# Performance work log

Hardware: AMD Instinct MI355X
Metric: run time of the kernel (lower is better)

Reference implementation:

```python
import jax, jax.numpy as jnp
import numpy as np

N_USER = 100000
N_ITEM = 100000
E = 800000
IN_USER, IN_ITEM, HID, OUT = 256, 128, 128, 64


def _gconv(x_src, W, b, src, dst, n_src, n_dst):
    """DGL GraphConv, norm='both', transform-before-aggregate (in>=out here)."""
    ones = jnp.ones(src.shape[0], x_src.dtype)
    deg_out = jax.ops.segment_sum(ones, src, num_segments=n_src)
    deg_in = jax.ops.segment_sum(ones, dst, num_segments=n_dst)
    inv_out = jnp.maximum(deg_out, 1.0) ** -0.5
    inv_in = jnp.maximum(deg_in, 1.0) ** -0.5
    x = (x_src @ W) * inv_out[:, None]            # [n_src, out]
    agg = jax.ops.segment_sum(x[src], dst, num_segments=n_dst)  # scatter-add over edges
    return agg * inv_in[:, None] + b


def setup_inputs() -> dict:
    key = jax.random.key(0)
    ks = jax.random.split(key, 24)
    d = {
        "feat_user": jax.random.normal(ks[0], (N_USER, IN_USER), jnp.float32),
        "feat_item": jax.random.normal(ks[1], (N_ITEM, IN_ITEM), jnp.float32),
        "rates_src": jax.random.randint(ks[2], (E,), 0, N_USER, jnp.int32),
        "rates_dst": jax.random.randint(ks[3], (E,), 0, N_ITEM, jnp.int32),
        "rated_src": jax.random.randint(ks[4], (E,), 0, N_ITEM, jnp.int32),
        "rated_dst": jax.random.randint(ks[5], (E,), 0, N_USER, jnp.int32),
        "fol_src": jax.random.randint(ks[6], (E,), 0, N_USER, jnp.int32),
        "fol_dst": jax.random.randint(ks[7], (E,), 0, N_USER, jnp.int32),
    }
    def glorot(k, shp):
        lim = np.sqrt(6.0 / (shp[0] + shp[1]))
        return jax.random.uniform(k, shp, jnp.float32, -lim, lim)
    d["W1_rates"] = glorot(ks[8], (IN_USER, HID)); d["b1_rates"] = jnp.zeros((HID,), jnp.float32)
    d["W1_rated"] = glorot(ks[9], (IN_ITEM, HID)); d["b1_rated"] = jnp.zeros((HID,), jnp.float32)
    d["W1_fol"] = glorot(ks[10], (IN_USER, HID)); d["b1_fol"] = jnp.zeros((HID,), jnp.float32)
    d["W2_rates"] = glorot(ks[11], (HID, OUT)); d["b2_rates"] = jnp.zeros((OUT,), jnp.float32)
    d["W2_rated"] = glorot(ks[12], (HID, OUT)); d["b2_rated"] = jnp.zeros((OUT,), jnp.float32)
    d["W2_fol"] = glorot(ks[13], (HID, OUT)); d["b2_fol"] = jnp.zeros((OUT,), jnp.float32)
    return d


def reference(feat_user, feat_item, rates_src, rates_dst, rated_src, rated_dst,
              fol_src, fol_dst, W1_rates, b1_rates, W1_rated, b1_rated,
              W1_fol, b1_fol, W2_rates, b2_rates, W2_rated, b2_rated,
              W2_fol, b2_fol):
    # layer 1 (HeteroGraphConv, sum-aggregate across relations per dst ntype)
    h_item = _gconv(feat_user, W1_rates, b1_rates, rates_src, rates_dst, N_USER, N_ITEM)
    h_user = (_gconv(feat_item, W1_rated, b1_rated, rated_src, rated_dst, N_ITEM, N_USER)
              + _gconv(feat_user, W1_fol, b1_fol, fol_src, fol_dst, N_USER, N_USER))
    # relu (dropout = identity in eval mode)
    h_user = jax.nn.relu(h_user)
    h_item = jax.nn.relu(h_item)
    # layer 2
    o_item = _gconv(h_user, W2_rates, b2_rates, rates_src, rates_dst, N_USER, N_ITEM)
    o_user = (_gconv(h_item, W2_rated, b2_rated, rated_src, rated_dst, N_ITEM, N_USER)
              + _gconv(h_user, W2_fol, b2_fol, fol_src, fol_dst, N_USER, N_USER))
    return jnp.stack([o_user, o_item])  # [2, N, OUT]
```

## Files before the change

### kernel.cpp

```cpp
#include <hip/hip_runtime.h>
#include <math.h>

#define IN_USER 256
#define IN_ITEM 128
#define HID 128
#define OUTF 64
#define NRANGE 8
#define NCHUNK 16
#define MAXRB 12544

typedef unsigned short u16;
typedef unsigned int u32;
typedef __attribute__((ext_vector_type(8))) __bf16 bf16x8;
typedef __attribute__((ext_vector_type(4))) float f32x4;

__device__ __forceinline__ u16 f2bf(float f) {
    union { float f; u32 u; } c; c.f = f;
    return (u16)((c.u + 0x7fffu + ((c.u >> 16) & 1u)) >> 16);
}
__device__ __forceinline__ u32 pack2(float a, float b) {
    return (u32)f2bf(a) | ((u32)f2bf(b) << 16);
}

__global__ __launch_bounds__(512) void hist_ranges(
        const int* __restrict__ a0, int e0, const int* __restrict__ a1, int e1,
        const int* __restrict__ a2, int e2, const int* __restrict__ a3, int e3,
        const int* __restrict__ a4, int e4, const int* __restrict__ a5, int e5,
        int* __restrict__ hist, int NP, int RB) {
    __shared__ int h[MAXRB];
    const int a = blockIdx.z;
    const int* arr; int E;
    switch (a) {
        case 0: arr = a0; E = e0; break;
        case 1: arr = a1; E = e1; break;
        case 2: arr = a2; E = e2; break;
        case 3: arr = a3; E = e3; break;
        case 4: arr = a4; E = e4; break;
        default: arr = a5; E = e5; break;
    }
    const int c = blockIdx.y;
    const int lo = blockIdx.x * RB;
    const u32 rbu = (u32)RB;
    const int tid = threadIdx.x;
    for (int i = tid; i < RB; i += 512) h[i] = 0;
    __syncthreads();
    const int ec = (((E + NCHUNK - 1) / NCHUNK) + 3) & ~3;
    const int s0 = c * ec;
    const int s1 = (s0 + ec) < E ? (s0 + ec) : E;
    if (s1 > s0) {
        const int n4 = (s1 - s0) >> 2;
        const int4* p4 = reinterpret_cast<const int4*>(arr + s0);
        for (int i = tid; i < n4; i += 512) {
            const int4 A = p4[i];
            u32 ux = (u32)(A.x - lo); if (ux < rbu) atomicAdd(&h[ux], 1);
            u32 uy = (u32)(A.y - lo); if (uy < rbu) atomicAdd(&h[uy], 1);
            u32 uz = (u32)(A.z - lo); if (uz < rbu) atomicAdd(&h[uz], 1);
            u32 uw = (u32)(A.w - lo); if (uw < rbu) atomicAdd(&h[uw], 1);
        }
        for (int j = s0 + (n4 << 2) + tid; j < s1; j += 512) {
            const u32 u = (u32)(arr[j] - lo);
            if (u < rbu) atomicAdd(&h[u], 1);
        }
    }
    __syncthreads();
    int* out = hist + ((size_t)a * NCHUNK + c) * NP + lo;
    for (int i = tid; i < RB; i += 512) out[i] = h[i];
}

__global__ __launch_bounds__(256) void hist_reduce(
        int* __restrict__ hist, int* __restrict__ deg,
        float* __restrict__ inv, int NP) {
    const int a = blockIdx.y;
    const int v = blockIdx.x * 256 + threadIdx.x;
    if (v >= NP) return;
    int* h = hist + (size_t)a * NCHUNK * NP + v;
    int s = 0;
#pragma unroll
    for (int c = 0; c < NCHUNK; ++c) {
        const int t = h[(size_t)c * NP];
        if (a & 1) h[(size_t)c * NP] = s;
        s += t;
    }
    deg[(size_t)a * NP + v] = s;
    inv[(size_t)a * NP + v] = 1.0f / sqrtf((float)(s > 1 ? s : 1));
}

__global__ __launch_bounds__(256) void scan_part(
        const int* __restrict__ d0, const int* __restrict__ d1,
        const int* __restrict__ d2, int n0, int n1, int n2,
        int* __restrict__ partial, int nblk) {
    const int rel = blockIdx.y;
    const int* deg = rel == 0 ? d0 : (rel == 1 ? d1 : d2);
    const int n = rel == 0 ? n0 : (rel == 1 ? n1 : n2);
    const int base = blockIdx.x * 1024 + threadIdx.x * 4;
    int s = 0;
#pragma unroll
    for (int i = 0; i < 4; ++i) {
        const int idx = base + i;
        if (idx < n) s += deg[idx];
    }
    __shared__ int red[256];
    red[threadIdx.x] = s;
    __syncthreads();
#pragma unroll
    for (int off = 128; off > 0; off >>= 1) {
        if (threadIdx.x < off) red[threadIdx.x] += red[threadIdx.x + off];
        __syncthreads();
    }
    if (threadIdx.x == 0) partial[rel * nblk + blockIdx.x] = red[0];
}

__global__ __launch_bounds__(128) void scan_mid(int* __restrict__ partial, int nblk) {
    __shared__ int sc[128];
    const int rel = blockIdx.x;
    const int t = threadIdx.x;
    const int v = (t < nblk) ? partial[rel * nblk + t] : 0;
    sc[t] = v;
    __syncthreads();
    for (int off = 1; off < 128; off <<= 1) {
        const int u = (t >= off) ? sc[t - off] : 0;
        __syncthreads();
        sc[t] += u;
        __syncthreads();
    }
    if (t < nblk) partial[rel * nblk + t] = sc[t] - v;
}

__global__ __launch_bounds__(256) void scan_final(
        const int* __restrict__ d0, const int* __restrict__ d1,
        const int* __restrict__ d2, int n0, int n1, int n2,
        const int* __restrict__ partial,
        int* __restrict__ c0, int* __restrict__ c1, int* __restrict__ c2,
        int nblk) {
    const int rel = blockIdx.y;
    const int* deg = rel == 0 ? d0 : (rel == 1 ? d1 : d2);
    int* cur = rel == 0 ? c0 : (rel == 1 ? c1 : c2);
    const int n = rel == 0 ? n0 : (rel == 1 ? n1 : n2);
    const int base = blockIdx.x * 1024 + threadIdx.x * 4;
    int v[4];
    int s = 0;
#pragma unroll
    for (int i = 0; i < 4; ++i) {
        const int idx = base + i;
        v[i] = (idx < n) ? deg[idx] : 0;
        s += v[i];
    }
    __shared__ int sc[256];
    sc[threadIdx.x] = s;
    __syncthreads();
    for (int off = 1; off < 256; off <<= 1) {
        const int u = (threadIdx.x >= off) ? sc[threadIdx.x - off] : 0;
        __syncthreads();
        sc[threadIdx.x] += u;
        __syncthreads();
    }
    int run = (threadIdx.x == 0 ? 0 : sc[threadIdx.x - 1]) + partial[rel * nblk + blockIdx.x];
#pragma unroll
    for (int i = 0; i < 4; ++i) {
        const int idx = base + i;
        if (idx < n) cur[idx] = run;
        run += v[i];
    }
}

__global__ __launch_bounds__(512) void fill_ranges(
        const int* __restrict__ s0p, const int* __restrict__ d0p, int e0,
        const int* __restrict__ s1p, const int* __restrict__ d1p, int e1,
        const int* __restrict__ s2p, const int* __restrict__ d2p, int e2,
        const int* __restrict__ cursor, const int* __restrict__ hist,
        int NP, int RB,
        int* __restrict__ csrbase, int off1, int off2) {
    __shared__ int cur[MAXRB];
    const int rel = blockIdx.z;
    const int* src = rel == 0 ? s0p : (rel == 1 ? s1p : s2p);
    const int* dst = rel == 0 ? d0p : (rel == 1 ? d1p : d2p);
    const int E = rel == 0 ? e0 : (rel == 1 ? e1 : e2);
    int* csr = csrbase + (rel == 0 ? 0 : (rel == 1 ? off1 : off2));
    const int c = blockIdx.y;
    const int lo = blockIdx.x * RB;
    const u32 rbu = (u32)RB;
    const int tid = threadIdx.x;
    const int* gc = cursor + (size_t)rel * NP + lo;
    const int* go = hist + ((size_t)(2 * rel + 1) * NCHUNK + c) * NP + lo;
    for (int i = tid; i < RB; i += 512) cur[i] = gc[i] + go[i];
    __syncthreads();
    const int ec = (((E + NCHUNK - 1) / NCHUNK) + 3) & ~3;
    const int s0 = c * ec;
    const int s1 = (s0 + ec) < E ? (s0 + ec) : E;
    if (s1 > s0) {
        const int n4 = (s1 - s0) >> 2;
        const int4* d4 = reinterpret_cast<const int4*>(dst + s0);
        const int4* s4 = reinterpret_cast<const int4*>(src + s0);
        for (int i = tid; i < n4; i += 512) {
            const int4 D = d4[i], S = s4[i];
            u32 ux = (u32)(D.x - lo); if (ux < rbu) { int p = atomicAdd(&cur[ux], 1); csr[p] = S.x; }
            u32 uy = (u32)(D.y - lo); if (uy < rbu) { int p = atomicAdd(&cur[uy], 1); csr[p] = S.y; }
            u32 uz = (u32)(D.z - lo); if (uz < rbu) { int p = atomicAdd(&cur[uz], 1); csr[p] = S.z; }
            u32 uw = (u32)(D.w - lo); if (uw < rbu) { int p = atomicAdd(&cur[uw], 1); csr[p] = S.w; }
        }
        for (int j = s0 + (n4 << 2) + tid; j < s1; j += 512) {
            const u32 u = (u32)(dst[j] - lo);
            if (u < rbu) { const int p = atomicAdd(&cur[u], 1); csr[p] = src[j]; }
        }
    }
}

__global__ __launch_bounds__(256) void wt_all(
        u16* __restrict__ Wt1u, const float* __restrict__ W1_rates,
        const float* __restrict__ W1_fol,
        u16* __restrict__ Wt1i, const float* __restrict__ W1_rated,
        u16* __restrict__ Wt2u, const float* __restrict__ W2_rates,
        const float* __restrict__ W2_fol,
        u16* __restrict__ Wt2i, const float* __restrict__ W2_rated) {
    int i = blockIdx.x * 256 + threadIdx.x;
    if (i < 65536) {
        const int n = i >> 8, k = i & 255;
        const float v = (n < 128) ? W1_rates[k * 128 + n] : W1_fol[k * 128 + (n - 128)];
        Wt1u[(size_t)n * 256 + k] = f2bf(v);
        return;
    }
    i -= 65536;
    if (i < 16384) {
        const int n = i >> 7, k = i & 127;
        Wt1i[(size_t)n * 128 + k] = f2bf(W1_rated[k * 128 + n]);
        return;
    }
    i -= 16384;
    if (i < 16384) {
        const int n = i >> 7, k = i & 127;
        const float v = (n < 64) ? W2_rates[k * 64 + n] : W2_fol[k * 64 + (n - 64)];
        Wt2u[(size_t)n * 128 + k] = f2bf(v);
        return;
    }
    i -= 16384;
    if (i < 8192) {
        const int n = i >> 7, k = i & 127;
        Wt2i[(size_t)n * 128 + k] = f2bf(W2_rated[k * 64 + n]);
    }
}

template<int WM, int WN, bool A_BF16>
__device__ __forceinline__ void gemm_body(
        u16* __restrict__ lbuf,
        const void* __restrict__ Xv, const u16* __restrict__ Wt,
        const float* __restrict__ invA, const float* __restrict__ invB,
        int nsplit, u16* __restrict__ T, int M, int TN, int K, int bx) {
    constexpr int BM = WM * 64, BN = WN * 64;
    constexpr int BLK = WM * WN * 64;
    constexpr int CA = 8 / WN;
    constexpr int CB = 8 / WM;
    u16* lA = lbuf;
    u16* lB = lbuf + BM * 64;
    const int tid = threadIdx.x;
    const int row0 = bx * BM;
    const int wid = tid >> 6, lane = tid & 63;
    const int wm = wid / WN, wn = wid % WN;
    const int l15 = lane & 15, lhi = lane >> 4;

    f32x4 acc[4][4] = {};

    for (int kk = 0; kk < K; kk += 64) {
        __syncthreads();
#pragma unroll
        for (int c = 0; c < CA; ++c) {
            const int cid = tid + c * BLK;
            const int row = cid >> 3, kc = cid & 7;
            const int grow = row0 + row;
            uint4 u = make_uint4(0, 0, 0, 0);
            if (A_BF16) {
                if (grow < M)
                    u = *reinterpret_cast<const uint4*>(
                        (const u16*)Xv + (size_t)grow * K + kk + kc * 8);
            } else {
                if (grow < M) {
                    const float* xp = (const float*)Xv + (size_t)grow * K + kk + kc * 8;
                    const float4 v0 = *reinterpret_cast<const float4*>(xp);
                    const float4 v1 = *reinterpret_cast<const float4*>(xp + 4);
                    u.x = pack2(v0.x, v0.y); u.y = pack2(v0.z, v0.w);
                    u.z = pack2(v1.x, v1.y); u.w = pack2(v1.z, v1.w);
                }
            }
            *reinterpret_cast<uint4*>(&lA[row * 64 + ((kc ^ (row & 7)) << 3)]) = u;
        }
#pragma unroll
        for (int c = 0; c < CB; ++c) {
            const int cid = tid + c * BLK;
            const int n = cid >> 3, kc = cid & 7;
            const uint4 u = *reinterpret_cast<const uint4*>(
                Wt + (size_t)n * K + kk + kc * 8);
            *reinterpret_cast<uint4*>(&lB[n * 64 + ((kc ^ (n & 7)) << 3)]) = u;
        }
        __syncthreads();
#pragma unroll
        for (int ks = 0; ks < 2; ++ks) {
            const int cb = ks * 4 + lhi;
            bf16x8 af[4], bfr[4];
#pragma unroll
            for (int fm = 0; fm < 4; ++fm) {
                const int r = wm * 64 + fm * 16 + l15;
                const uint4 u = *reinterpret_cast<const uint4*>(
                    &lA[r * 64 + ((cb ^ (r & 7)) << 3)]);
                af[fm] = __builtin_bit_cast(bf16x8, u);
            }
#pragma unroll
            for (int fn = 0; fn < 4; ++fn) {
                const int r = wn * 64 + fn * 16 + l15;
                const uint4 u = *reinterpret_cast<const uint4*>(
                    &lB[r * 64 + ((cb ^ (r & 7)) << 3)]);
                bfr[fn] = __builtin_bit_cast(bf16x8, u);
            }
#pragma unroll
            for (int fm = 0; fm < 4; ++fm)
#pragma unroll
                for (int fn = 0; fn < 4; ++fn)
                    acc[fm][fn] = __builtin_amdgcn_mfma_f32_16x16x32_bf16(
                        af[fm], bfr[fn], acc[fm][fn], 0, 0, 0);
        }
    }

    const int colw = wn * 64;
    const float* invp = (colw >= nsplit) ? invB : invA;
#pragma unroll
    for (int fm = 0; fm < 4; ++fm) {
#pragma unroll
        for (int r4 = 0; r4 < 4; ++r4) {
            const int grow = row0 + wm * 64 + fm * 16 + lhi * 4 + r4;
            if (grow < M) {
                const float s = invp[grow];
#pragma unroll
                for (int fn = 0; fn < 4; ++fn) {
                    const int col = colw + fn * 16 + l15;
                    T[(size_t)grow * TN + col] = f2bf(acc[fm][fn][r4] * s);
                }
            }
        }
    }
}

__global__ __launch_bounds__(256) void gemm_l1(
        const float* __restrict__ Xu, const u16* __restrict__ Wt1u,
        const float* __restrict__ Xi, const u16* __restrict__ Wt1i,
        const float* __restrict__ inv0, const float* __restrict__ inv4,
        const float* __restrict__ inv2,
        u16* __restrict__ t1u, u16* __restrict__ t1i,
        int nU, int nI, int gbI) {
    __shared__ u16 lbuf[20480];
    if (blockIdx.y == 0) {
        gemm_body<1, 4, false>(lbuf, Xu, Wt1u, inv0, inv4, 128, t1u, nU, 256, 256, blockIdx.x);
    } else {
        if ((int)blockIdx.x >= gbI) return;
        gemm_body<2, 2, false>(lbuf, Xi, Wt1i, inv2, inv2, 1 << 30, t1i, nI, 128, 128, blockIdx.x);
    }
}

__global__ __launch_bounds__(256) void gemm_l2(
        const u16* __restrict__ aggU, const u16* __restrict__ Wt2u,
        const u16* __restrict__ aggI, const u16* __restrict__ Wt2i,
        const float* __restrict__ inv0, const float* __restrict__ inv4,
        const float* __restrict__ inv2,
        u16* __restrict__ t2u, u16* __restrict__ t2i,
        int nU, int nI, int gbI) {
    __shared__ u16 lbuf[20480];
    if (blockIdx.y == 0) {
        gemm_body<2, 2, true>(lbuf, aggU, Wt2u, inv0, inv4, 64, t2u, nU, 128, 128, blockIdx.x);
    } else {
        if ((int)blockIdx.x >= gbI) return;
        gemm_body<4, 1, true>(lbuf, aggI, Wt2i, inv2, inv2, 1 << 30, t2i, nI, 64, 128, blockIdx.x);
    }
}

template<int F>
__device__ __forceinline__ void gather_rel(
        const u16* __restrict__ T, int strideT, int offT,
        const int* __restrict__ csr, int beg, int cnt, int Z, int lane,
        float& s0, float& s1) {
    const int* cp = csr + beg;
    const int loff = (F == 128) ? lane * 2 : lane;
    for (int e = 0; e < cnt; e += 8) {
        int idx[8];
#pragma unroll
        for (int i = 0; i < 8; ++i) {
            const int t = cp[e + i];
            idx[i] = __builtin_amdgcn_readfirstlane((e + i < cnt) ? t : Z);
        }
        if (F == 128) {
            u32 v[8];
#pragma unroll
            for (int i = 0; i < 8; ++i)
                v[i] = *reinterpret_cast<const u32*>(
                    T + (size_t)idx[i] * strideT + offT + loff);
#pragma unroll
            for (int i = 0; i < 8; ++i) {
                union { u32 u; float f; } lo, hi;
                lo.u = v[i] << 16;
                hi.u = v[i] & 0xffff0000u;
                s0 += lo.f; s1 += hi.f;
            }
        } else {
            u16 v[8];
#pragma unroll
            for (int i = 0; i < 8; ++i)
                v[i] = T[(size_t)idx[i] * strideT + offT + loff];
#pragma unroll
            for (int i = 0; i < 8; ++i) {
                union { u32 u; float f; } c;
                c.u = ((u32)v[i]) << 16;
                s0 += c.f;
            }
        }
    }
}

template<int F, bool TWO, bool RELU, bool BF16OUT>
__device__ __forceinline__ void gather_node(
        const u16* __restrict__ Ta, int strideA, int offA,
        const int* __restrict__ csrA, const int* __restrict__ curA,
        const int* __restrict__ degA, const float* __restrict__ invA,
        const float* __restrict__ biasA,
        const u16* __restrict__ Tb, int strideB, int offB,
        const int* __restrict__ csrB, const int* __restrict__ curB,
        const int* __restrict__ degB, const float* __restrict__ invB,
        const float* __restrict__ biasB,
        void* __restrict__ outv, int Z, int wid, int lane) {
    float r0, r1 = 0.f;
    {
        const int cnt = degA[wid];
        const int beg = curA[wid];
        float s0 = 0.f, s1 = 0.f;
        gather_rel<F>(Ta, strideA, offA, csrA, beg, cnt, Z, lane, s0, s1);
        const float a = invA[wid];
        if (F == 128) {
            const float2 b = *reinterpret_cast<const float2*>(biasA + lane * 2);
            r0 = s0 * a + b.x; r1 = s1 * a + b.y;
        } else {
            r0 = s0 * a + biasA[lane];
        }
    }
    if (TWO) {
        const int cnt = degB[wid];
        const int beg = curB[wid];
        float s0 = 0.f, s1 = 0.f;
        gather_rel<F>(Tb, strideB, offB, csrB, beg, cnt, Z, lane, s0, s1);
        const float a = invB[wid];
        if (F == 128) {
            const float2 b = *reinterpret_cast<const float2*>(biasB + lane * 2);
            r0 += s0 * a + b.x; r1 += s1 * a + b.y;
        } else {
            r0 += s0 * a + biasB[lane];
        }
    }
    if (RELU) { r0 = fmaxf(r0, 0.f); r1 = fmaxf(r1, 0.f); }
    if (BF16OUT) {
        if (F == 128)
            ((u32*)outv)[(size_t)wid * 64 + lane] = pack2(r0, r1);
        else
            ((u16*)outv)[(size_t)wid * 64 + lane] = f2bf(r0);
    } else {
        if (F == 128) {
            float2 o; o.x = r0; o.y = r1;
            *reinterpret_cast<float2*>((float*)outv + (size_t)wid * 128 + lane * 2) = o;
        } else {
            ((float*)outv)[(size_t)wid * 64 + lane] = r0;
        }
    }
}

__global__ __launch_bounds__(256) void gather_l1(
        const u16* __restrict__ t1u, const u16* __restrict__ t1i,
        const int* __restrict__ csr0, const int* __restrict__ cur0,
        const int* __restrict__ deg1, const float* __restrict__ inv1,
        const float* __restrict__ b1_rates,
        const int* __restrict__ csr1, const int* __restrict__ cur1,
        const int* __restrict__ deg3, const float* __restrict__ inv3,
        const float* __restrict__ b1_rated,
        const int* __restrict__ csr2, const int* __restrict__ cur2,
        const int* __restrict__ deg5, const float* __restrict__ inv5,
        const float* __restrict__ b1_fol,
        u16* __restrict__ aggI, u16* __restrict__ aggU,
        int Z, int nI, int nU) {
    const int wid = (blockIdx.x * 256 + threadIdx.x) >> 6;
    const int lane = threadIdx.x & 63;
    if (blockIdx.y == 0) {
        if (wid >= nI) return;
        gather_node<128, false, true, true>(
            t1u, 256, 0, csr0, cur0, deg1, inv1, b1_rates,
            nullptr, 0, 0, nullptr, nullptr, nullptr, nullptr, nullptr,
            aggI, Z, wid, lane);
    } else {
        if (wid >= nU) return;
        gather_node<128, true, true, true>(
            t1i, 128, 0, csr1, cur1, deg3, inv3, b1_rated,
            t1u, 256, 128, csr2, cur2, deg5, inv5, b1_fol,
            aggU, Z, wid, lane);
    }
}

__global__ __launch_bounds__(256) void gather_l2(
        const u16* __restrict__ t2u, const u16* __restrict__ t2i,
        const int* __restrict__ csr0, const int* __restrict__ cur0,
        const int* __restrict__ deg1, const float* __restrict__ inv1,
        const float* __restrict__ b2_rates,
        const int* __restrict__ csr1, const int* __restrict__ cur1,
        const int* __restrict__ deg3, const float* __restrict__ inv3,
        const float* __restrict__ b2_rated,
        const int* __restrict__ csr2, const int* __restrict__ cur2,
        const int* __restrict__ deg5, const float* __restrict__ inv5,
        const float* __restrict__ b2_fol,
        float* __restrict__ o_item, float* __restrict__ o_user,
        int Z, int nI, int nU) {
    const int wid = (blockIdx.x * 256 + threadIdx.x) >> 6;
    const int lane = threadIdx.x & 63;
    if (blockIdx.y == 0) {
        if (wid >= nI) return;
        gather_node<64, false, false, false>(
            t2u, 128, 0, csr0, cur0, deg1, inv1, b2_rates,
            nullptr, 0, 0, nullptr, nullptr, nullptr, nullptr, nullptr,
            o_item, Z, wid, lane);
    } else {
        if (wid >= nU) return;
        gather_node<64, true, false, false>(
            t2i, 64, 0, csr1, cur1, deg3, inv3, b2_rated,
            t2u, 128, 64, csr2, cur2, deg5, inv5, b2_fol,
            o_user, Z, wid, lane);
    }
}

extern "C" void kernel_launch(void* const* d_in, const int* in_sizes, int n_in,
                              void* d_out, int out_size, void* d_ws, size_t ws_size,
                              hipStream_t stream) {
    const float* feat_user = (const float*)d_in[0];
    const float* feat_item = (const float*)d_in[1];
    const int* rates_src = (const int*)d_in[2];
    const int* rates_dst = (const int*)d_in[3];
    const int* rated_src = (const int*)d_in[4];
    const int* rated_dst = (const int*)d_in[5];
    const int* fol_src   = (const int*)d_in[6];
    const int* fol_dst   = (const int*)d_in[7];
    const float* W1_rates = (const float*)d_in[8];
    const float* b1_rates = (const float*)d_in[9];
    const float* W1_rated = (const float*)d_in[10];
    const float* b1_rated = (const float*)d_in[11];
    const float* W1_fol   = (const float*)d_in[12];
    const float* b1_fol   = (const float*)d_in[13];
    const float* W2_rates = (const float*)d_in[14];
    const float* b2_rates = (const float*)d_in[15];
    const float* W2_rated = (const float*)d_in[16];
    const float* b2_rated = (const float*)d_in[17];
    const float* W2_fol   = (const float*)d_in[18];
    const float* b2_fol   = (const float*)d_in[19];

    const int n_user = in_sizes[0] / IN_USER;
    const int n_item = in_sizes[1] / IN_ITEM;
    const int E0 = in_sizes[2];
    const int E1 = in_sizes[4];
    const int E2 = in_sizes[6];
    const int nmax = n_user > n_item ? n_user : n_item;
    const int Z = nmax;

    const size_t NP = ((size_t)(nmax + 1023) / 1024) * 1024;
    int*   deg     = (int*)d_ws;
    float* inv     = (float*)(deg + 6 * NP);
    int*   cursor  = (int*)(inv + 6 * NP);
    int*   partial = cursor + 3 * NP;
    int*   csr  = partial + 3 * 128;
    int*   csr0 = csr;
    int*   csr1 = csr + E0;
    int*   csr2 = csr + E0 + E1;
    u16* Wt1u = (u16*)(csr + E0 + E1 + E2);
    u16* Wt1i = Wt1u + 256 * 256;
    u16* Wt2u = Wt1i + 128 * 128;
    u16* Wt2i = Wt2u + 128 * 128;
    u16* t1u  = Wt2i + 64 * 128;
    u16* t1i  = t1u + (size_t)(nmax + 1) * 256;
    u16* aggU = t1i + (size_t)(nmax + 1) * 128;
    u16* aggI = aggU + (size_t)nmax * 128;
    u16* t2u  = t1i;
    u16* t2i  = t1u;
    int* hist = (int*)t1u;

    float* o_user = (float*)d_out;
    float* o_item = o_user + (size_t)n_user * OUTF;

    hipMemsetAsync(t1u + (size_t)Z * 256, 0, 512, stream);
    hipMemsetAsync(t1i + (size_t)Z * 128, 0, 256, stream);

    const int RB = (int)(NP / NRANGE);
    hist_ranges<<<dim3(NRANGE, NCHUNK, 6), 512, 0, stream>>>(
        rates_src, E0, rates_dst, E0, rated_src, E1,
        rated_dst, E1, fol_src, E2, fol_dst, E2, hist, (int)NP, RB);
    hist_reduce<<<dim3((int)(NP + 255) / 256, 6), 256, 0, stream>>>(
        hist, deg, inv, (int)NP);

    wt_all<<<(65536 + 16384 + 16384 + 8192 + 255) / 256, 256, 0, stream>>>(
        Wt1u, W1_rates, W1_fol, Wt1i, W1_rated,
        Wt2u, W2_rates, W2_fol, Wt2i, W2_rated);

    const int nblk = (int)(NP / 1024);
    scan_part<<<dim3(nblk, 3), 256, 0, stream>>>(
        deg + 1 * NP, deg + 3 * NP, deg + 5 * NP, n_item, n_user, n_user, partial, nblk);
    scan_mid<<<3, 128, 0, stream>>>(partial, nblk);
    scan_final<<<dim3(nblk, 3), 256, 0, stream>>>(
        deg + 1 * NP, deg + 3 * NP, deg + 5 * NP, n_item, n_user, n_user, partial,
        cursor + 0 * NP, cursor + 1 * NP, cursor + 2 * NP, nblk);
    fill_ranges<<<dim3(NRANGE, NCHUNK, 3), 512, 0, stream>>>(
        rates_src, rates_dst, E0, rated_src, rated_dst, E1,
        fol_src, fol_dst, E2, cursor, hist, (int)NP, RB, csr, E0, E0 + E1);

    const int gbU1 = (n_user + 63) / 64;
    const int gbI1 = (n_item + 127) / 128;
    const int gbU2 = (n_user + 127) / 128;
    const int gbI2 = (n_item + 255) / 256;
    const int gw   = (nmax * 64 + 255) / 256;

    gemm_l1<<<dim3(gbU1, 2), 256, 0, stream>>>(
        feat_user, Wt1u, feat_item, Wt1i,
        inv + 0 * NP, inv + 4 * NP, inv + 2 * NP,
        t1u, t1i, n_user, n_item, gbI1);

    gather_l1<<<dim3(gw, 2), 256, 0, stream>>>(
        t1u, t1i,
        csr0, cursor + 0 * NP, deg + 1 * NP, inv + 1 * NP, b1_rates,
        csr1, cursor + 1 * NP, deg + 3 * NP, inv + 3 * NP, b1_rated,
        csr2, cursor + 2 * NP, deg + 5 * NP, inv + 5 * NP, b1_fol,
        aggI, aggU, Z, n_item, n_user);

    hipMemsetAsync(t2i + (size_t)Z * 64, 0, 128, stream);

    gemm_l2<<<dim3(gbU2, 2), 256, 0, stream>>>(
        aggU, Wt2u, aggI, Wt2i,
        inv + 0 * NP, inv + 4 * NP, inv + 2 * NP,
        t2u, t2i, n_user, n_item, gbI2);

    gather_l2<<<dim3(gw, 2), 256, 0, stream>>>(
        t2u, t2i,
        csr0, cursor + 0 * NP, deg + 1 * NP, inv + 1 * NP, b2_rates,
        csr1, cursor + 1 * NP, deg + 3 * NP, inv + 3 * NP, b2_rated,
        csr2, cursor + 2 * NP, deg + 5 * NP, inv + 5 * NP, b2_fol,
        o_item, o_user, Z, n_item, n_user);
}
```

Before: 399.3 us.

## Merge CSR fill and layer-1 GEMM into one concurrent launch

Folds the fill_ranges CSR construction kernel into the layer-1 GEMM launch, so that the fill work (grid y<3) and the user/item GEMMs (y=3,4) run as blocks of one 5-row grid and overlap. The GEMM tiles grow to 512-thread blocks covering 128 and 256 rows, with gemm_body now templated on the thread count. The histogram scratch moves from the t1u buffer to aggU so it no longer aliases the GEMM output being written at the same time. This saves one launch and the idle tail between the two phases, at the cost of larger LDS use per block (about 49 KB), which may reduce occupancy, and many early-exit blocks in the padded grid.

Measured after the change: 404.5 us. No clear change (+1.3%).

```diff
diff --git a/kernel.cpp b/kernel.cpp
--- a/kernel.cpp
+++ b/kernel.cpp
@@ -163,48 +163,6 @@
     }
 }
 
-__global__ __launch_bounds__(512) void fill_ranges(
-        const int* __restrict__ s0p, const int* __restrict__ d0p, int e0,
-        const int* __restrict__ s1p, const int* __restrict__ d1p, int e1,
-        const int* __restrict__ s2p, const int* __restrict__ d2p, int e2,
-        const int* __restrict__ cursor, const int* __restrict__ hist,
-        int NP, int RB,
-        int* __restrict__ csrbase, int off1, int off2) {
-    __shared__ int cur[MAXRB];
-    const int rel = blockIdx.z;
-    const int* src = rel == 0 ? s0p : (rel == 1 ? s1p : s2p);
-    const int* dst = rel == 0 ? d0p : (rel == 1 ? d1p : d2p);
-    const int E = rel == 0 ? e0 : (rel == 1 ? e1 : e2);
-    int* csr = csrbase + (rel == 0 ? 0 : (rel == 1 ? off1 : off2));
-    const int c = blockIdx.y;
-    const int lo = blockIdx.x * RB;
-    const u32 rbu = (u32)RB;
-    const int tid = threadIdx.x;
-    const int* gc = cursor + (size_t)rel * NP + lo;
-    const int* go = hist + ((size_t)(2 * rel + 1) * NCHUNK + c) * NP + lo;
-    for (int i = tid; i < RB; i += 512) cur[i] = gc[i] + go[i];
-    __syncthreads();
-    const int ec = (((E + NCHUNK - 1) / NCHUNK) + 3) & ~3;
-    const int s0 = c * ec;
-    const int s1 = (s0 + ec) < E ? (s0 + ec) : E;
-    if (s1 > s0) {
-        const int n4 = (s1 - s0) >> 2;
-        const int4* d4 = reinterpret_cast<const int4*>(dst + s0);
-        const int4* s4 = reinterpret_cast<const int4*>(src + s0);
-        for (int i = tid; i < n4; i += 512) {
-            const int4 D = d4[i], S = s4[i];
-            u32 ux = (u32)(D.x - lo); if (ux < rbu) { int p = atomicAdd(&cur[ux], 1); csr[p] = S.x; }
-            u32 uy = (u32)(D.y - lo); if (uy < rbu) { int p = atomicAdd(&cur[uy], 1); csr[p] = S.y; }
-            u32 uz = (u32)(D.z - lo); if (uz < rbu) { int p = atomicAdd(&cur[uz], 1); csr[p] = S.z; }
-            u32 uw = (u32)(D.w - lo); if (uw < rbu) { int p = atomicAdd(&cur[uw], 1); csr[p] = S.w; }
-        }
-        for (int j = s0 + (n4 << 2) + tid; j < s1; j += 512) {
-            const u32 u = (u32)(dst[j] - lo);
-            if (u < rbu) { const int p = atomicAdd(&cur[u], 1); csr[p] = src[j]; }
-        }
-    }
-}
-
 __global__ __launch_bounds__(256) void wt_all(
         u16* __restrict__ Wt1u, const float* __restrict__ W1_rates,
         const float* __restrict__ W1_fol,
@@ -239,16 +197,16 @@
     }
 }
 
-template<int WM, int WN, bool A_BF16>
+template<int NT, int WM, int WN, bool A_BF16>
 __device__ __forceinline__ void gemm_body(
         u16* __restrict__ lbuf,
         const void* __restrict__ Xv, const u16* __restrict__ Wt,
         const float* __restrict__ invA, const float* __restrict__ invB,
         int nsplit, u16* __restrict__ T, int M, int TN, int K, int bx) {
     constexpr int BM = WM * 64, BN = WN * 64;
-    constexpr int BLK = WM * WN * 64;
-    constexpr int CA = 8 / WN;
-    constexpr int CB = 8 / WM;
+    constexpr int CA = BM * 8 / NT;
+    constexpr int CB = BN * 8 / NT;
+    static_assert(NT == WM * WN * 64, "wave grid mismatch");
     u16* lA = lbuf;
     u16* lB = lbuf + BM * 64;
     const int tid = threadIdx.x;
@@ -263,7 +221,7 @@
         __syncthreads();
 #pragma unroll
         for (int c = 0; c < CA; ++c) {
-            const int cid = tid + c * BLK;
+            const int cid = tid + c * NT;
             const int row = cid >> 3, kc = cid & 7;
             const int grow = row0 + row;
             uint4 u = make_uint4(0, 0, 0, 0);
@@ -284,7 +242,7 @@
         }
 #pragma unroll
         for (int c = 0; c < CB; ++c) {
-            const int cid = tid + c * BLK;
+            const int cid = tid + c * NT;
             const int n = cid >> 3, kc = cid & 7;
             const uint4 u = *reinterpret_cast<const uint4*>(
                 Wt + (size_t)n * K + kk + kc * 8);
@@ -337,19 +295,64 @@
     }
 }
 
-__global__ __launch_bounds__(256) void gemm_l1(
+__global__ __launch_bounds__(512) void mega_l1(
+        const int* __restrict__ s0p, const int* __restrict__ d0p, int e0,
+        const int* __restrict__ s1p, const int* __restrict__ d1p, int e1,
+        const int* __restrict__ s2p, const int* __restrict__ d2p, int e2,
+        const int* __restrict__ cursor, const int* __restrict__ hist,
+        int NP, int RB, int* __restrict__ csrbase, int off1, int off2,
         const float* __restrict__ Xu, const u16* __restrict__ Wt1u,
         const float* __restrict__ Xi, const u16* __restrict__ Wt1i,
         const float* __restrict__ inv0, const float* __restrict__ inv4,
         const float* __restrict__ inv2,
         u16* __restrict__ t1u, u16* __restrict__ t1i,
-        int nU, int nI, int gbI) {
-    __shared__ u16 lbuf[20480];
-    if (blockIdx.y == 0) {
-        gemm_body<1, 4, false>(lbuf, Xu, Wt1u, inv0, inv4, 128, t1u, nU, 256, 256, blockIdx.x);
+        int nU, int nI, int gbU, int gbI) {
+    __shared__ __align__(16) char smem[50176];
+    const int y = blockIdx.y;
+    const int x = blockIdx.x;
+    if (y < 3) {
+        if (x >= NRANGE * NCHUNK) return;
+        int* cur = (int*)smem;
+        const int rel = y;
+        const int* src = rel == 0 ? s0p : (rel == 1 ? s1p : s2p);
+        const int* dst = rel == 0 ? d0p : (rel == 1 ? d1p : d2p);
+        const int E = rel == 0 ? e0 : (rel == 1 ? e1 : e2);
+        int* csr = csrbase + (rel == 0 ? 0 : (rel == 1 ? off1 : off2));
+        const int rng = x >> 4, c = x & 15;
+        const int lo = rng * RB;
+        const u32 rbu = (u32)RB;
+        const int tid = threadIdx.x;
+        const int* gc = cursor + (size_t)rel * NP + lo;
+        const int* go = hist + ((size_t)(2 * rel + 1) * NCHUNK + c) * NP + lo;
+        for (int i = tid; i < RB; i += 512) cur[i] = gc[i] + go[i];
+        __syncthreads();
+        const int ec = (((E + NCHUNK - 1) / NCHUNK) + 3) & ~3;
+        const int s0 = c * ec;
+        const int s1 = (s0 + ec) < E ? (s0 + ec) : E;
+        if (s1 > s0) {
+            const int n4 = (s1 - s0) >> 2;
+            const int4* d4 = reinterpret_cast<const int4*>(dst + s0);
+            const int4* s4 = reinterpret_cast<const int4*>(src + s0);
+            for (int i = tid; i < n4; i += 512) {
+                const int4 D = d4[i], S = s4[i];
+                u32 ux = (u32)(D.x - lo); if (ux < rbu) { int p = atomicAdd(&cur[ux], 1); csr[p] = S.x; }
+                u32 uy = (u32)(D.y - lo); if (uy < rbu) { int p = atomicAdd(&cur[uy], 1); csr[p] = S.y; }
+                u32 uz = (u32)(D.z - lo); if (uz < rbu) { int p = atomicAdd(&cur[uz], 1); csr[p] = S.z; }
+                u32 uw = (u32)(D.w - lo); if (uw < rbu) { int p = atomicAdd(&cur[uw], 1); csr[p] = S.w; }
+            }
+            for (int j = s0 + (n4 << 2) + tid; j < s1; j += 512) {
+                const u32 u = (u32)(dst[j] - lo);
+                if (u < rbu) { const int p = atomicAdd(&cur[u], 1); csr[p] = src[j]; }
+            }
+        }
+    } else if (y == 3) {
+        if (x >= gbU) return;
+        gemm_body<512, 2, 4, false>((u16*)smem, Xu, Wt1u, inv0, inv4, 128,
+                                    t1u, nU, 256, 256, x);
     } else {
-        if ((int)blockIdx.x >= gbI) return;
-        gemm_body<2, 2, false>(lbuf, Xi, Wt1i, inv2, inv2, 1 << 30, t1i, nI, 128, 128, blockIdx.x);
+        if (x >= gbI) return;
+        gemm_body<512, 4, 2, false>((u16*)smem, Xi, Wt1i, inv2, inv2, 1 << 30,
+                                    t1i, nI, 128, 128, x);
     }
 }
 
@@ -362,10 +365,10 @@
         int nU, int nI, int gbI) {
     __shared__ u16 lbuf[20480];
     if (blockIdx.y == 0) {
-        gemm_body<2, 2, true>(lbuf, aggU, Wt2u, inv0, inv4, 64, t2u, nU, 128, 128, blockIdx.x);
+        gemm_body<256, 2, 2, true>(lbuf, aggU, Wt2u, inv0, inv4, 64, t2u, nU, 128, 128, blockIdx.x);
     } else {
         if ((int)blockIdx.x >= gbI) return;
-        gemm_body<4, 1, true>(lbuf, aggI, Wt2i, inv2, inv2, 1 << 30, t2i, nI, 64, 128, blockIdx.x);
+        gemm_body<256, 4, 1, true>(lbuf, aggI, Wt2i, inv2, inv2, 1 << 30, t2i, nI, 64, 128, blockIdx.x);
     }
 }
 
@@ -576,7 +579,7 @@
     u16* aggI = aggU + (size_t)nmax * 128;
     u16* t2u  = t1i;
     u16* t2i  = t1u;
-    int* hist = (int*)t1u;
+    int* hist = (int*)aggU;
 
     float* o_user = (float*)d_out;
     float* o_item = o_user + (size_t)n_user * OUTF;
@@ -602,20 +605,20 @@
     scan_final<<<dim3(nblk, 3), 256, 0, stream>>>(
         deg + 1 * NP, deg + 3 * NP, deg + 5 * NP, n_item, n_user, n_user, partial,
         cursor + 0 * NP, cursor + 1 * NP, cursor + 2 * NP, nblk);
-    fill_ranges<<<dim3(NRANGE, NCHUNK, 3), 512, 0, stream>>>(
-        rates_src, rates_dst, E0, rated_src, rated_dst, E1,
-        fol_src, fol_dst, E2, cursor, hist, (int)NP, RB, csr, E0, E0 + E1);
-
-    const int gbU1 = (n_user + 63) / 64;
-    const int gbI1 = (n_item + 127) / 128;
+
+    const int gbU1 = (n_user + 127) / 128;
+    const int gbI1 = (n_item + 255) / 256;
     const int gbU2 = (n_user + 127) / 128;
     const int gbI2 = (n_item + 255) / 256;
+    const int megax = gbU1 > (NRANGE * NCHUNK) ? gbU1 : (NRANGE * NCHUNK);
     const int gw   = (nmax * 64 + 255) / 256;
 
-    gemm_l1<<<dim3(gbU1, 2), 256, 0, stream>>>(
+    mega_l1<<<dim3(megax, 5), 512, 0, stream>>>(
+        rates_src, rates_dst, E0, rated_src, rated_dst, E1,
+        fol_src, fol_dst, E2, cursor, hist, (int)NP, RB, csr, E0, E0 + E1,
         feat_user, Wt1u, feat_item, Wt1i,
         inv + 0 * NP, inv + 4 * NP, inv + 2 * NP,
-        t1u, t1i, n_user, n_item, gbI1);
+        t1u, t1i, n_user, n_item, gbU1, gbI1);
 
     gather_l1<<<dim3(gw, 2), 256, 0, stream>>>(
         t1u, t1i,
```
